# Performance work log

Measured on AMD Instinct MI355X. Metric: run time of the kernel, lower is better.

The kernel has to match this reference:

```python
import jax, jax.numpy as jnp
import numpy as np

DIM = 512
HEADS = 16
HD = DIM // HEADS            # head_dim = 32
WH, WW = 8, 8                # window_size
D0, D1 = 2, 2                # dilated_size
TWH, TWW = WH * D0, WW * D1  # total_window_size = 16,16
SCALE = HD ** -0.5


def _wpart(x, wh, ww):
    # (B,H,W,C) -> (B * H/wh * W/ww, wh, ww, C)
    B, H, W, C = x.shape
    x = x.reshape(B, H // wh, wh, W // ww, ww, C)
    return x.transpose(0, 1, 3, 2, 4, 5).reshape(-1, wh, ww, C)


def _wrev(win, wh, ww, H, W):
    # (nW*B, wh, ww, C) -> (B, H, W, C)
    C = win.shape[-1]
    B = win.shape[0] // ((H // wh) * (W // ww))
    x = win.reshape(B, H // wh, W // ww, wh, ww, C).transpose(0, 1, 3, 2, 4, 5)
    return x.reshape(B, H, W, C)


def _rope2(x):
    # 2D RoPE over a (B, WH, WW, HD) window: first half of HD rotated by row
    # position, second half by column position (axial rotary embedding).
    d = HD // 2
    inv = 1.0 / (10000.0 ** (jnp.arange(0, d, 2, dtype=jnp.float32) / d))  # (d/2,)

    def rot(xp, ang):
        x1, x2 = xp[..., 0::2], xp[..., 1::2]
        c, s = jnp.cos(ang), jnp.sin(ang)
        return jnp.stack([x1 * c - x2 * s, x1 * s + x2 * c], axis=-1).reshape(xp.shape)

    ah = (jnp.arange(WH, dtype=jnp.float32)[:, None] * inv)[:, None, :]  # (WH,1,d/2)
    aw = (jnp.arange(WW, dtype=jnp.float32)[:, None] * inv)[None, :, :]  # (1,WW,d/2)
    return jnp.concatenate([rot(x[..., :d], ah), rot(x[..., d:], aw)], axis=-1)


def _forward(x, qkv_w, qkv_b, proj_w, proj_b):
    B, H, W, C = x.shape
    # partition into total windows, then dilated regrouping
    xw = _wpart(x, TWH, TWW)                                   # (B_, 16, 16, C)
    B_ = xw.shape[0]
    xw = _wpart(xw, D0, D1)                                    # (B_*64, 2, 2, C)
    xw = xw.reshape(B_, WH * WW, D0 * D1, C)
    xw = xw.transpose(0, 2, 1, 3).reshape(B_ * D0 * D1, WH * WW, C)  # (B__, N, C)
    B__, N = xw.shape[0], xw.shape[1]

    qkv = (xw @ qkv_w.T + qkv_b).reshape(B__, N, 3, HEADS, HD).transpose(2, 0, 3, 1, 4)
    q, k, v = qkv[0], qkv[1], qkv[2]                           # (B__, HEADS, N, HD)

    q = _rope2(q.reshape(-1, WH, WW, HD)).reshape(B__, HEADS, N, HD) * SCALE
    k = _rope2(k.reshape(-1, WH, WW, HD)).reshape(B__, HEADS, N, HD)

    attn = jax.nn.softmax(jnp.einsum('bhnd,bhmd->bhnm', q, k), axis=-1)
    out = jnp.einsum('bhnm,bhmd->bhnd', attn, v)               # (B__, HEADS, N, HD)
    out = out.transpose(0, 2, 1, 3).reshape(B__, N, C)

    # undo dilated regrouping, then undo total-window partition
    out = out.reshape(B_, D0 * D1, N, C).transpose(0, 2, 1, 3).reshape(-1, D0, D1, C)
    out = _wrev(out, D0, D1, TWH, TWW)                         # (B_, 16, 16, C)
    out = _wrev(out, TWH, TWW, H, W)                           # (B, H, W, C)
    return out @ proj_w.T + proj_b


def setup_inputs() -> dict:
    key = jax.random.key(0)
    k0, k1, k2 = jax.random.split(key, 3)
    x = jax.random.normal(k0, (4, 128, 128, DIM), dtype=jnp.float32)
    qkv_w = jax.random.normal(k1, (3 * DIM, DIM), dtype=jnp.float32) * (DIM ** -0.5)
    qkv_b = jnp.zeros((3 * DIM,), dtype=jnp.float32)
    proj_w = jax.random.normal(k2, (DIM, DIM), dtype=jnp.float32) * (DIM ** -0.5)
    proj_b = jnp.zeros((DIM,), dtype=jnp.float32)
    return {"x": x, "qkv_w": qkv_w, "qkv_b": qkv_b, "proj_w": proj_w, "proj_b": proj_b}


def reference(x, qkv_w, qkv_b, proj_w, proj_b):
    return _forward(x, qkv_w, qkv_b, proj_w, proj_b)
```

## Files before the change

### kernel.cpp

```cpp
#include <hip/hip_runtime.h>
#include <hip/hip_bf16.h>
#include <stdint.h>

#define DIMC  512
#define NHEAD 16
#define HDIM  32
#define NTOK  65536
#define QKVN  1536
static constexpr float SCALE_F = 0.17677669529663687f;

typedef __attribute__((ext_vector_type(4))) float  f32x4;
typedef __attribute__((ext_vector_type(8))) __bf16 bf16x8;

__device__ __forceinline__ uint16_t f2bf(float f) {
  union { float f; uint32_t u; } v; v.f = f;
  return (uint16_t)((v.u + 0x7FFFu + ((v.u >> 16) & 1u)) >> 16);
}

__device__ __forceinline__ void gload_lds16(const void* g, void* l) {
  __builtin_amdgcn_global_load_lds((const __attribute__((address_space(1))) void*)g,
                                   (__attribute__((address_space(3))) void*)l,
                                   16, 0, 0);
}

__global__ void cvt_f32_bf16(const float* __restrict__ src,
                             uint16_t* __restrict__ dst, int n4)
{
  int i = blockIdx.x * blockDim.x + threadIdx.x;
  const int stride = gridDim.x * blockDim.x;
  for (; i < n4; i += stride) {
    const float4 v = ((const float4*)src)[i];
    ushort4 o;
    o.x = f2bf(v.x); o.y = f2bf(v.y); o.z = f2bf(v.z); o.w = f2bf(v.w);
    ((ushort4*)dst)[i] = o;
  }
}

template <bool OUT_F32>
__global__ __launch_bounds__(512, 2)
void gemm256_8ph(const uint16_t* __restrict__ A,
                 const uint16_t* __restrict__ B,
                 const float* __restrict__ bias,
                 void* __restrict__ Cv,
                 int M, int N, int K, int gx)
{
  __shared__ __align__(16) char lds[131072];

  const int tid = threadIdx.x;
  const int l  = tid & 63, w = tid >> 6;
  const int wm = w >> 2,  wn = w & 3;
  const int lm = l & 15,  lq = l >> 4;

  const int nwg = gridDim.x;
  const int qq = nwg >> 3, rr = nwg & 7;
  const int xcd = blockIdx.x & 7, loc = blockIdx.x >> 3;
  const int sw = (xcd < rr ? xcd * (qq + 1) : rr * (qq + 1) + (xcd - rr) * qq) + loc;
  const long m0 = (long)(sw / gx) * 256;
  const long n0 = (long)(sw % gx) * 256;

  const int srow  = tid >> 3;
  const int scolb = (((tid & 7) ^ (srow & 7)) << 4);
  const uint16_t* Ags = A + (m0 + srow) * (long)K + (scolb >> 1);
  const uint16_t* Bgs = B + (n0 + srow) * (long)K + (scolb >> 1);
  char* ldsW = lds + (w << 10);

#define STAGE(Gs, regionOff, half, kt)                                        \
  {                                                                           \
    const uint16_t* s0_ = (Gs) + (size_t)((half) * 128) * K + (kt);           \
    gload_lds16(s0_,                  ldsW + (regionOff));                    \
    gload_lds16(s0_ + (size_t)64 * K, ldsW + (regionOff) + 8192);             \
  }

  const int colx0 = ((lq ^ (lm & 7)) << 4);
  const int aoff0 = (wm * 64 + lm) * 128 + colx0;
  const int aoff1 = (wm * 64 + lm) * 128 + (colx0 ^ 64);
  const int boff0 = (wn * 32 + lm) * 128 + colx0;
  const int boff1 = (wn * 32 + lm) * 128 + (colx0 ^ 64);

  f32x4  acc[2][2][4][2] = {};
  bf16x8 aX[4][2], aY[4][2];
  bf16x8 b0[2][2], b1[2][2];

#define RD_A(DST, OFF)                                                        \
  _Pragma("unroll") for (int i = 0; i < 4; ++i) {                             \
    DST[i][0] = *(const bf16x8*)(lds + (OFF) + aoff0 + i * 2048);             \
    DST[i][1] = *(const bf16x8*)(lds + (OFF) + aoff1 + i * 2048);             \
  }
#define RD_B(DST, OFF)                                                        \
  _Pragma("unroll") for (int j = 0; j < 2; ++j) {                             \
    DST[j][0] = *(const bf16x8*)(lds + (OFF) + boff0 + j * 2048);             \
    DST[j][1] = *(const bf16x8*)(lds + (OFF) + boff1 + j * 2048);             \
  }
#define MFMA16(AS, BS, QM, QN)                                                \
  __builtin_amdgcn_s_setprio(1);                                              \
  _Pragma("unroll") for (int kk = 0; kk < 2; ++kk)                            \
    _Pragma("unroll") for (int i = 0; i < 4; ++i)                             \
      _Pragma("unroll") for (int j = 0; j < 2; ++j)                           \
        acc[QM][QN][i][j] = __builtin_amdgcn_mfma_f32_16x16x32_bf16(          \
            AS[i][kk], BS[j][kk], acc[QM][QN][i][j], 0, 0, 0);                \
  __builtin_amdgcn_s_setprio(0);
#define VMW(N) asm volatile("s_waitcnt vmcnt(" #N ")" ::: "memory");
#define BAR()  asm volatile("s_barrier" ::: "memory");

  STAGE(Ags, 0,             0, 0)
  STAGE(Bgs, 32768,         0, 0)
  STAGE(Ags, 16384,         1, 0)
  STAGE(Bgs, 49152,         1, 0)
  STAGE(Ags, 65536,         0, 64)
  STAGE(Bgs, 65536 + 32768, 0, 64)
  VMW(8) BAR()
  RD_A(aX, 0) RD_B(b0, 32768)
  VMW(4) BAR()

  for (int t2 = 0; t2 < K / 64; t2 += 2) {
    const int k1 = (t2 + 1) * 64;
    int k2 = (t2 + 2) * 64; if (k2 >= K) k2 = 0;
    int k3 = (t2 + 3) * 64; if (k3 >= K) k3 = 0;

    RD_B(b1, 49152)                 STAGE(Ags, 65536 + 16384, 1, k1)
    MFMA16(aX, b0, 0, 0)            BAR()
    RD_A(aY, 16384)                 STAGE(Bgs, 65536 + 49152, 1, k1)
    MFMA16(aX, b1, 0, 1)            BAR()
    STAGE(Ags, 0, 0, k2)
    MFMA16(aY, b0, 1, 0)            VMW(6) BAR()
    RD_A(aX, 65536) RD_B(b0, 65536 + 32768)
    STAGE(Bgs, 32768, 0, k2)
    MFMA16(aY, b1, 1, 1)            VMW(4) BAR()
    RD_B(b1, 65536 + 49152)         STAGE(Ags, 16384, 1, k2)
    MFMA16(aX, b0, 0, 0)            BAR()
    RD_A(aY, 65536 + 16384)         STAGE(Bgs, 49152, 1, k2)
    MFMA16(aX, b1, 0, 1)            BAR()
    STAGE(Ags, 65536, 0, k3)
    MFMA16(aY, b0, 1, 0)            VMW(6) BAR()
    RD_A(aX, 0) RD_B(b0, 32768)
    STAGE(Bgs, 65536 + 32768, 0, k3)
    MFMA16(aY, b1, 1, 1)            VMW(4) BAR()
  }
#undef STAGE
#undef RD_A
#undef RD_B
#undef MFMA16
#undef VMW
#undef BAR

#pragma unroll
  for (int qm = 0; qm < 2; ++qm)
#pragma unroll
  for (int qn = 0; qn < 2; ++qn)
#pragma unroll
  for (int i = 0; i < 4; ++i)
#pragma unroll
  for (int j = 0; j < 2; ++j) {
    const long m = m0 + qm * 128 + wm * 64 + i * 16 + lq * 4;
    const long n = n0 + qn * 128 + wn * 32 + j * 16 + lm;
    const float bv = bias[n];
#pragma unroll
    for (int r = 0; r < 4; ++r) {
      const float val = acc[qm][qn][i][j][r] + bv;
      if (OUT_F32) ((float*)Cv)[(m + r) * (long)N + n] = val;
      else         ((uint16_t*)Cv)[(m + r) * (long)N + n] = f2bf(val);
    }
  }
}

__global__ void attn_win(const uint16_t* __restrict__ QKV,
                         uint16_t* __restrict__ O)
{
  __shared__ __align__(16) __bf16 Pl[4][64][72];

  const int tid = threadIdx.x;
  const int l  = tid & 63, w = tid >> 6;
  const int lm = l & 15,  lq = l >> 4;
  const int bid = blockIdx.x;
  const int g = bid >> 2;
  const int h = (bid & 3) * 4 + w;

  const int d1 = g & 1, d0 = (g >> 1) & 1;
  const int wx = (g >> 2) & 7, wy = (g >> 5) & 7, bb = g >> 8;
  const long tbase = ((long)(bb * 128 + wy * 16 + d0) * 128) + wx * 16 + d1;

  f32x4 invs;
#pragma unroll
  for (int i = 0; i < 4; ++i)
    invs[i] = exp2f(-1.6609640474436813f * (float)((lq & 1) * 4 + i));

  const int co_q = h * HDIM;
  const int co_k = DIMC + h * HDIM;
  const int co_v = 2 * DIMC + h * HDIM;

  bf16x8 qf[4], kf[4];
#pragma unroll
  for (int f = 0; f < 4; ++f) {
    const int n  = f * 16 + lm;
    const int iy = n >> 3, ix = n & 7;
    const float pos = (lq < 2) ? (float)iy : (float)ix;
    const long t = tbase + iy * 256 + ix * 2;
    const uint16_t* qp = QKV + t * QKVN + co_q + lq * 8;
    const uint16_t* kp = QKV + t * QKVN + co_k + lq * 8;
    {
      bf16x8 raw = *(const bf16x8*)qp, o;
#pragma unroll
      for (int i = 0; i < 4; ++i) {
        float x1 = (float)raw[2 * i], x2 = (float)raw[2 * i + 1];
        float s, c; __sincosf(pos * invs[i], &s, &c);
        o[2 * i]     = (__bf16)((x1 * c - x2 * s) * SCALE_F);
        o[2 * i + 1] = (__bf16)((x1 * s + x2 * c) * SCALE_F);
      }
      qf[f] = o;
    }
    {
      bf16x8 raw = *(const bf16x8*)kp, o;
#pragma unroll
      for (int i = 0; i < 4; ++i) {
        float x1 = (float)raw[2 * i], x2 = (float)raw[2 * i + 1];
        float s, c; __sincosf(pos * invs[i], &s, &c);
        o[2 * i]     = (__bf16)(x1 * c - x2 * s);
        o[2 * i + 1] = (__bf16)(x1 * s + x2 * c);
      }
      kf[f] = o;
    }
  }

  const f32x4 fzero = {0.f, 0.f, 0.f, 0.f};
  f32x4 s[4][4];
#pragma unroll
  for (int mi = 0; mi < 4; ++mi)
#pragma unroll
    for (int ni = 0; ni < 4; ++ni)
      s[mi][ni] = __builtin_amdgcn_mfma_f32_16x16x32_bf16(qf[mi], kf[ni], fzero, 0, 0, 0);

  float rsum[4][4];
#pragma unroll
  for (int mi = 0; mi < 4; ++mi)
#pragma unroll
    for (int r = 0; r < 4; ++r) {
      float m = s[mi][0][r];
#pragma unroll
      for (int ni = 1; ni < 4; ++ni) m = fmaxf(m, s[mi][ni][r]);
      m = fmaxf(m, __shfl_xor(m, 1));
      m = fmaxf(m, __shfl_xor(m, 2));
      m = fmaxf(m, __shfl_xor(m, 4));
      m = fmaxf(m, __shfl_xor(m, 8));
      float sum = 0.f;
#pragma unroll
      for (int ni = 0; ni < 4; ++ni) {
        float p = expf(s[mi][ni][r] - m);
        s[mi][ni][r] = p;
        sum += p;
      }
      sum += __shfl_xor(sum, 1);
      sum += __shfl_xor(sum, 2);
      sum += __shfl_xor(sum, 4);
      sum += __shfl_xor(sum, 8);
      rsum[mi][r] = sum;
    }

#pragma unroll
  for (int mi = 0; mi < 4; ++mi)
#pragma unroll
    for (int ni = 0; ni < 4; ++ni)
#pragma unroll
      for (int r = 0; r < 4; ++r)
        Pl[w][mi * 16 + lq * 4 + r][ni * 16 + lm] = (__bf16)s[mi][ni][r];

  bf16x8 pa[4][2];
#pragma unroll
  for (int mi = 0; mi < 4; ++mi)
#pragma unroll
    for (int kk = 0; kk < 2; ++kk)
      pa[mi][kk] = *(const bf16x8*)(&Pl[w][mi * 16 + lm][kk * 32 + lq * 8]);

  bf16x8 vf[2][2];
#pragma unroll
  for (int kk = 0; kk < 2; ++kk)
#pragma unroll
    for (int n2 = 0; n2 < 2; ++n2) {
      const int nb = kk * 32 + lq * 8;
      const long tb2 = tbase + (long)(nb >> 3) * 256;
      const uint16_t* vp = QKV + co_v + n2 * 16 + lm;
      bf16x8 o;
#pragma unroll
      for (int i = 0; i < 8; ++i)
        o[i] = *(const __bf16*)(vp + (tb2 + 2 * i) * QKVN);
      vf[kk][n2] = o;
    }

  f32x4 oacc[4][2] = {};
#pragma unroll
  for (int kk = 0; kk < 2; ++kk)
#pragma unroll
    for (int mi = 0; mi < 4; ++mi)
#pragma unroll
      for (int n2 = 0; n2 < 2; ++n2)
        oacc[mi][n2] = __builtin_amdgcn_mfma_f32_16x16x32_bf16(
            pa[mi][kk], vf[kk][n2], oacc[mi][n2], 0, 0, 0);

#pragma unroll
  for (int mi = 0; mi < 4; ++mi)
#pragma unroll
    for (int r = 0; r < 4; ++r) {
      const int n = mi * 16 + lq * 4 + r;
      const long t = tbase + (n >> 3) * 256 + (n & 7) * 2;
      const float rinv = 1.0f / rsum[mi][r];
#pragma unroll
      for (int n2 = 0; n2 < 2; ++n2)
        O[t * DIMC + h * HDIM + n2 * 16 + lm] = f2bf(oacc[mi][n2][r] * rinv);
    }
}

extern "C" void kernel_launch(void* const* d_in, const int* in_sizes, int n_in,
                              void* d_out, int out_size, void* d_ws, size_t ws_size,
                              hipStream_t stream)
{
  const float* x      = (const float*)d_in[0];
  const float* qkv_w  = (const float*)d_in[1];
  const float* qkv_b  = (const float*)d_in[2];
  const float* proj_w = (const float*)d_in[3];
  const float* proj_b = (const float*)d_in[4];
  float* out = (float*)d_out;

  uint16_t* xb   = (uint16_t*)d_ws;
  uint16_t* qwb  = xb  + (size_t)NTOK * DIMC;
  uint16_t* pwb  = qwb + (size_t)QKVN * DIMC;
  uint16_t* qkv  = pwb + (size_t)DIMC * DIMC;
  uint16_t* attn = qkv + (size_t)NTOK * QKVN;

  cvt_f32_bf16<<<2048, 256, 0, stream>>>(x,      xb,  NTOK * DIMC / 4);
  cvt_f32_bf16<<<512,  256, 0, stream>>>(qkv_w,  qwb, QKVN * DIMC / 4);
  cvt_f32_bf16<<<256,  256, 0, stream>>>(proj_w, pwb, DIMC * DIMC / 4);

  gemm256_8ph<false><<<dim3((NTOK / 256) * (QKVN / 256)), dim3(512), 0, stream>>>(
      xb, qwb, qkv_b, qkv, NTOK, QKVN, DIMC, QKVN / 256);

  attn_win<<<dim3(1024 * 4), dim3(256), 0, stream>>>(qkv, attn);

  gemm256_8ph<true><<<dim3((NTOK / 256) * (DIMC / 256)), dim3(512), 0, stream>>>(
      attn, pwb, proj_b, out, NTOK, DIMC, DIMC, DIMC / 256);
}
```

Before: 298.4 us.

## Use 128x128 single-buffered DMA GEMM kernel for QKV projection

Adds a new GEMM kernel with 128x128 tiles, 256 threads and four waves, and uses it for the QKV projection in place of the 256x256 eight-phase kernel. Tiles are loaded with global_load_lds into an XOR-swizzled LDS layout and multiplied with bf16 16x16x32 MFMA. The kernel is single-buffered, with two barriers per K step and no overlap between loads and MFMA. The smaller tile uses less LDS and allows more resident workgroups, at the cost of lower data reuse per tile and more global traffic.

```diff
diff --git a/kernel.cpp b/kernel.cpp
--- a/kernel.cpp
+++ b/kernel.cpp
@@ -34,6 +34,87 @@
     o.x = f2bf(v.x); o.y = f2bf(v.y); o.z = f2bf(v.z); o.w = f2bf(v.w);
     ((ushort4*)dst)[i] = o;
   }
+}
+
+template <bool OUT_F32>
+__global__ __launch_bounds__(256, 4)
+void gemm128_dma(const uint16_t* __restrict__ A,
+                 const uint16_t* __restrict__ B,
+                 const float* __restrict__ bias,
+                 void* __restrict__ Cv,
+                 int M, int N, int K, int gx)
+{
+  __shared__ __align__(16) __bf16 As[128][64];
+  __shared__ __align__(16) __bf16 Bs[128][64];
+
+  const int tid = threadIdx.x;
+  const int l  = tid & 63, w = tid >> 6;
+  const int wm = w >> 1,  wn = w & 1;
+  const int lm = l & 15,  lq = l >> 4;
+
+  const int nwg = gridDim.x;
+  const int qq = nwg >> 3, rr = nwg & 7;
+  const int xcd = blockIdx.x & 7, loc = blockIdx.x >> 3;
+  const int sw = (xcd < rr ? xcd * (qq + 1) : rr * (qq + 1) + (xcd - rr) * qq) + loc;
+  const long m0 = (long)(sw / gx) * 128;
+  const long n0 = (long)(sw % gx) * 128;
+
+  const int dr = w * 8 + (l >> 3);
+  const int su = (l & 7) ^ ((l >> 3) & 7);
+  const uint16_t* Ag = A + (m0 + dr) * (long)K + su * 8;
+  const uint16_t* Bg = B + (n0 + dr) * (long)K + su * 8;
+  char* AsC = (char*)&As[0][0];
+  char* BsC = (char*)&Bs[0][0];
+
+  f32x4 acc[4][4] = {};
+
+  for (int kt = 0; kt < K; kt += 64) {
+    __syncthreads();
+#pragma unroll
+    for (int c = 0; c < 4; ++c) {
+      gload_lds16(Ag + (size_t)c * 32 * K + kt, AsC + w * 1024 + c * 4096);
+      gload_lds16(Bg + (size_t)c * 32 * K + kt, BsC + w * 1024 + c * 4096);
+    }
+    __syncthreads();
+
+#pragma unroll
+    for (int kk = 0; kk < 2; ++kk) {
+      bf16x8 a[4], b[4];
+#pragma unroll
+      for (int i = 0; i < 4; ++i)
+        a[i] = *(const bf16x8*)(AsC + (wm * 64 + i * 16 + lm) * 128 +
+                                (((kk * 4 + lq) ^ (lm & 7)) << 4));
+#pragma unroll
+      for (int i = 0; i < 4; ++i)
+        b[i] = *(const bf16x8*)(BsC + (wn * 64 + i * 16 + lm) * 128 +
+                                (((kk * 4 + lq) ^ (lm & 7)) << 4));
+#pragma unroll
+      for (int mi = 0; mi < 4; ++mi)
+#pragma unroll
+        for (int ni = 0; ni < 4; ++ni)
+          acc[mi][ni] = __builtin_amdgcn_mfma_f32_16x16x32_bf16(
+              a[mi], b[ni], acc[mi][ni], 0, 0, 0);
+    }
+  }
+
+  float bvals[4];
+#pragma unroll
+  for (int ni = 0; ni < 4; ++ni)
+    bvals[ni] = bias[n0 + wn * 64 + ni * 16 + lm];
+
+#pragma unroll
+  for (int mi = 0; mi < 4; ++mi)
+#pragma unroll
+    for (int ni = 0; ni < 4; ++ni) {
+      const long m = m0 + wm * 64 + mi * 16 + lq * 4;
+      const long n = n0 + wn * 64 + ni * 16 + lm;
+#pragma unroll
+      for (int r = 0; r < 4; ++r) {
+        const float val = acc[mi][ni][r] + bvals[ni];
+        if (OUT_F32) ((float*)Cv)[(m + r) * (long)N + n] = val;
+        else         ((uint16_t*)Cv)[(m + r) * (long)N + n] = f2bf(val);
+      }
+    }
 }
 
 template <bool OUT_F32>
@@ -329,8 +410,8 @@
   cvt_f32_bf16<<<512,  256, 0, stream>>>(qkv_w,  qwb, QKVN * DIMC / 4);
   cvt_f32_bf16<<<256,  256, 0, stream>>>(proj_w, pwb, DIMC * DIMC / 4);
 
-  gemm256_8ph<false><<<dim3((NTOK / 256) * (QKVN / 256)), dim3(512), 0, stream>>>(
-      xb, qwb, qkv_b, qkv, NTOK, QKVN, DIMC, QKVN / 256);
+  gemm128_dma<false><<<dim3((NTOK / 128) * (QKVN / 128)), dim3(256), 0, stream>>>(
+      xb, qwb, qkv_b, qkv, NTOK, QKVN, DIMC, QKVN / 128);
 
   attn_win<<<dim3(1024 * 4), dim3(256), 0, stream>>>(qkv, attn);
 
```

After: 300.1 us. About the same (+0.6%).
